# Optimization experiments

Hardware: AMD Instinct MI355X
Metric: run time of the kernel (lower is better)

Reference implementation:

```python
import jax, jax.numpy as jnp
import numpy as np

B, S, E, D = 8, 2048, 1024, 64


def setup_inputs() -> dict:
    key = jax.random.key(0)
    ks = jax.random.split(key, 8)
    x = jax.random.normal(ks[0], (B, S, E), dtype=jnp.float32)
    mask = jax.random.randint(ks[1], (B, S), 0, 2, dtype=jnp.int32)
    # torch.nn.Linear(E, D): weight [D, E], bias [D]; y = x @ W.T + b
    scale = 0.02
    Wq = jax.random.normal(ks[2], (D, E), dtype=jnp.float32) * scale
    bq = jax.random.normal(ks[3], (D,), dtype=jnp.float32) * scale
    Wk = jax.random.normal(ks[4], (D, E), dtype=jnp.float32) * scale
    bk = jax.random.normal(ks[5], (D,), dtype=jnp.float32) * scale
    Wv = jax.random.normal(ks[6], (D, E), dtype=jnp.float32) * scale
    bv = jax.random.normal(ks[7], (D,), dtype=jnp.float32) * scale
    return {"x": x, "mask": mask, "Wq": Wq, "bq": bq, "Wk": Wk, "bk": bk, "Wv": Wv, "bv": bv}


def reference(x, mask, Wq, bq, Wk, bk, Wv, bv):
    # Linear projections: [B,S,E] @ [E,D] -> [B,S,D]
    q = jnp.einsum('bse,de->bsd', x, Wq) + bq
    k = jnp.einsum('bse,de->bsd', x, Wk) + bk
    v = jnp.einsum('bse,de->bsd', x, Wv) + bv
    # scores: [B,S,S]
    scores = jnp.einsum('bid,bjd->bij', q, k) / np.sqrt(D).astype(np.float32)
    # Faithful mask replication: temp_mask[b,i,j] = mask[b,j] if j >= i else 0;
    # positions where temp_mask == 0 are filled with -1e22 (training=True).
    seq = scores.shape[1]
    upper = jnp.triu(jnp.ones((seq, seq), dtype=bool))        # j >= i
    valid = upper[None, :, :] & (mask[:, None, :] != 0)        # [B,S,S]
    scores = jnp.where(valid, scores, jnp.float32(-1e22))
    attn = jax.nn.softmax(scores, axis=-1)
    # out: [B,S,D]
    return jnp.einsum('bij,bjd->bid', attn, v)
```

## Files before the change

kernel.cpp:

```cpp
#include <hip/hip_runtime.h>
#include <hip/hip_bf16.h>

#define NB 8
#define NS 2048
#define NE 1024
#define ND 64

typedef __attribute__((ext_vector_type(8))) short bf16x8;
typedef __attribute__((ext_vector_type(4))) float f32x4;
typedef unsigned short u16;
typedef unsigned long long u64;

#define MFMA(a, b, c) __builtin_amdgcn_mfma_f32_16x16x32_bf16(a, b, c, 0, 0, 0)
#define KEEPB(n) asm volatile("s_waitcnt vmcnt(" #n ")\n\ts_barrier" ::: "memory")

__device__ __forceinline__ u16 f2bf(float f) {
  unsigned int u = __float_as_uint(f);
  u += 0x7fffu + ((u >> 16) & 1u);
  return (u16)(u >> 16);
}
__device__ __forceinline__ unsigned cvt2(float a, float b) {
  __hip_bfloat162 h = __float22bfloat162_rn(float2{a, b});
  return *(unsigned*)&h;
}

__device__ __forceinline__ void alds16(const void* g, void* l) {
  __builtin_amdgcn_global_load_lds(
      (const __attribute__((address_space(1))) unsigned int*)g,
      (__attribute__((address_space(3))) unsigned int*)l, 16, 0, 0);
}

__global__ void k0_prep(const float* __restrict__ Wq, const float* __restrict__ bq,
                        const float* __restrict__ Wk, const float* __restrict__ bk,
                        const float* __restrict__ Wv, const float* __restrict__ bv,
                        u16* __restrict__ Wcat3, float* __restrict__ bcat,
                        float* __restrict__ vmean) {
  int d = blockIdx.x * 256 + threadIdx.x;
  int c = d / 768;
  int rem = d - c * 768;
  int n = rem >> 2;
  int v = rem & 3;
  const float* src = (n < 64) ? (Wq + n * NE) : (n < 128) ? (Wk + (n - 64) * NE)
                                                          : (Wv + (n - 128) * NE);
  const float* sp = src + c * 32 + v * 8;
  float4 a = *(const float4*)sp;
  float4 b = *(const float4*)(sp + 4);
  bf16x8 o;
  o[0] = (short)f2bf(a.x); o[1] = (short)f2bf(a.y);
  o[2] = (short)f2bf(a.z); o[3] = (short)f2bf(a.w);
  o[4] = (short)f2bf(b.x); o[5] = (short)f2bf(b.y);
  o[6] = (short)f2bf(b.z); o[7] = (short)f2bf(b.w);
  *(bf16x8*)&Wcat3[(size_t)d * 8] = o;
  if (blockIdx.x == 0) {
    int t = threadIdx.x;
    if (t < 192) bcat[t] = (t < 64) ? bq[t] : (t < 128) ? bk[t - 64] : bv[t - 128];
    vmean[t] = 0.f;
    vmean[t + 256] = 0.f;
  }
}

__global__ __launch_bounds__(512) void k1_qkv(
    const float* __restrict__ x, const u16* __restrict__ Wcat3,
    const float* __restrict__ bcat, u16* __restrict__ qb,
    u16* __restrict__ kbf2, u16* __restrict__ vtb2, float* __restrict__ vmean) {
  __shared__ float axs[4][1024];
  __shared__ u16 bsb[4][6144];
  const int t = threadIdx.x;
  const int m0 = blockIdx.x * 32;
  const int batch = m0 >> 11;
  const int sl = m0 & (NS - 1);
  const int w = t >> 6;
  const int l = t & 63;
  const int ln = l & 15;
  const int qd = l >> 4;
  const int rg = w & 1;
  const int cg = w >> 1;

  f32x4 zf = {0.f, 0.f, 0.f, 0.f};
  f32x4 acc[3] = {zf, zf, zf};

  auto stage = [&](int c, int buf) {
    if (w < 2) {
      #pragma unroll
      for (int i = 0; i < 2; ++i) {
        int un = w * 128 + i * 64 + l;
        int row = un >> 3;
        int q = (un & 7) ^ (row & 7);
        alds16(x + (size_t)(m0 + row) * NE + c * 32 + q * 4,
               &axs[buf][(w * 128 + i * 64) * 4]);
      }
    } else {
      #pragma unroll
      for (int i = 0; i < 2; ++i) {
        int ub = (w - 2) * 128 + i * 64 + l;
        int n = ub >> 2;
        int v = (ub & 3) ^ ((n ^ (n >> 2)) & 3);
        alds16(Wcat3 + (size_t)c * 6144 + n * 32 + v * 8,
               &bsb[buf][((w - 2) * 128 + i * 64) * 8]);
      }
    }
  };

  auto comp = [&](int buf) {
    const int arow = rg * 16 + ln;
    const int s = arow & 7;
    float4 fa = *(const float4*)&axs[buf][arow * 32 + (((qd * 2) ^ s) << 2)];
    float4 fb = *(const float4*)&axs[buf][arow * 32 + (((qd * 2 + 1) ^ s) << 2)];
    union { bf16x8 v; unsigned u[4]; } A;
    A.u[0] = cvt2(fa.x, fa.y); A.u[1] = cvt2(fa.z, fa.w);
    A.u[2] = cvt2(fb.x, fb.y); A.u[3] = cvt2(fb.z, fb.w);
    #pragma unroll
    for (int nj = 0; nj < 3; ++nj) {
      int n = cg * 48 + nj * 16 + ln;
      int sw = (n ^ (n >> 2)) & 3;
      bf16x8 bb = *(const bf16x8*)&bsb[buf][n * 32 + ((qd ^ sw) << 3)];
      acc[nj] = MFMA(A.v, bb, acc[nj]);
    }
  };

  stage(0, 0);
  stage(1, 1);
  stage(2, 2);
  for (int c = 0; c < 29; ++c) {
    KEEPB(4);
    stage(c + 3, (c + 3) & 3);
    comp(c & 3);
  }
  KEEPB(4); comp(1);
  KEEPB(2); comp(2);
  KEEPB(0); comp(3);

  const float QS = 0.125f;
  #pragma unroll
  for (int nj = 0; nj < 3; ++nj) {
    int n = cg * 48 + nj * 16 + ln;
    float bias = bcat[n];
    int jbase = sl + rg * 16 + qd * 4;
    if (n < 64) {
      #pragma unroll
      for (int r = 0; r < 4; ++r)
        qb[((size_t)batch * NS + jbase + r) * ND + n] = f2bf((acc[nj][r] + bias) * QS);
    } else if (n < 128) {
      int d = n - 64;
      #pragma unroll
      for (int r = 0; r < 4; ++r) {
        int j = jbase + r;
        int pos = (((d >> 3) ^ (j & 7)) << 3) + (d & 7);
        kbf2[((size_t)batch * NS + j) * ND + pos] = f2bf(acc[nj][r] + bias);
      }
    } else {
      int d = n - 128;
      int off = (jbase & ~63) + (((((jbase >> 5) & 1) ^ ((d >> 2) & 1))) << 5) +
                (((((jbase >> 3) & 3) ^ (d & 3))) << 3) + (jbase & 7);
      ushort4 sv;
      sv.x = f2bf(acc[nj][0] + bias); sv.y = f2bf(acc[nj][1] + bias);
      sv.z = f2bf(acc[nj][2] + bias); sv.w = f2bf(acc[nj][3] + bias);
      *(ushort4*)&vtb2[((size_t)batch * ND + d) * NS + off] = sv;
      float psum = acc[nj][0] + acc[nj][1] + acc[nj][2] + acc[nj][3] + 4.f * bias;
      psum += __shfl_xor(psum, 16);
      psum += __shfl_xor(psum, 32);
      if (l < 16) atomicAdd(&vmean[batch * ND + d], psum * (1.f / 2048.f));
    }
  }
}

__global__ __launch_bounds__(512) void k3_attn(
    const u16* __restrict__ qb, const u16* __restrict__ kbf2,
    const u16* __restrict__ vtb2, const int* __restrict__ mask,
    const float* __restrict__ vmean, float* __restrict__ out) {
  __shared__ u16 ks[2][128 * 64];
  __shared__ u16 vs[2][64 * 128];
  __shared__ union {
    u16 ps[8][16 * 40];
    struct { float mb[2][16][68]; float mlb[2][16][16]; } m;
  } ub;

  const int g = blockIdx.x;
  const int b = g & 7;
  const int uu = g >> 3;
  const int tile = (uu & 1) ? (63 - (uu >> 1)) : (uu >> 1);
  const int i0 = tile * 32;
  const int j0f = i0 & ~127;
  const int np = (NS - j0f) >> 7;
  const int t = threadIdx.x;
  const int w = t >> 6;
  const int l = t & 63;
  const int ln = l & 15;
  const int qd = l >> 4;
  const int rg = w & 1;
  const int jg = w >> 1;

  const u16* qp = qb + ((size_t)b * NS + i0 + rg * 16 + ln) * ND + qd * 8;
  bf16x8 aq0 = *(const bf16x8*)qp;
  bf16x8 aq1 = *(const bf16x8*)(qp + 32);

  const u16* kB = kbf2 + (size_t)b * NS * ND;
  const u16* vB = vtb2 + (size_t)b * ND * NS;

  auto stage = [&](int it, int buf) {
    int j0 = j0f + it * 128;
    #pragma unroll
    for (int i = 0; i < 2; ++i) {
      int jl = w * 16 + i * 8;
      alds16(kB + (size_t)(j0 + jl) * ND + l * 8, &ks[buf][jl * 64]);
      int du = w * 2 + i;
      alds16(vB + (size_t)(du * 4 + (l >> 4)) * NS + j0 + (l & 15) * 8,
             &vs[buf][du * 512]);
    }
  };

  f32x4 zf = {0.f, 0.f, 0.f, 0.f};
  f32x4 od[4] = {zf, zf, zf, zf};
  float ls[4] = {0.f, 0.f, 0.f, 0.f};
  const int pvunit = (jg >> 1) * 8 + (((jg & 1) ^ ((ln >> 2) & 1)) << 2) + (qd ^ (ln & 3));

  stage(0, 0);
  int mval = mask[b * NS + j0f + jg * 32 + (l & 31)];

  auto body = [&](int it, bool causal) {
    u64 mv = __ballot(mval != 0);
    __syncthreads();
    if (it + 1 < np) {
      stage(it + 1, (it + 1) & 1);
      mval = mask[b * NS + j0f + (it + 1) * 128 + jg * 32 + (l & 31)];
    }
    const int buf = it & 1;
    const int jb = j0f + it * 128 + jg * 32;

    f32x4 sc[2] = {zf, zf};
    #pragma unroll
    for (int f = 0; f < 2; ++f) {
      const u16* kr = &ks[buf][(jg * 32 + f * 16 + ln) * 64];
      bf16x8 b0 = *(const bf16x8*)&kr[((qd ^ (ln & 7)) * 8)];
      bf16x8 b1 = *(const bf16x8*)&kr[(((4 + qd) ^ (ln & 7)) * 8)];
      sc[f] = MFMA(aq0, b0, sc[f]);
      sc[f] = MFMA(aq1, b1, sc[f]);
    }
    #pragma unroll
    for (int r = 0; r < 4; ++r) {
      const int i = i0 + rg * 16 + qd * 4 + r;
      #pragma unroll
      for (int f = 0; f < 2; ++f) {
        int jl = f * 16 + ln;
        bool ok = (((mv >> jl) & 1ull) != 0) && (!causal || (jb + jl >= i));
        float p = ok ? __expf(sc[f][r]) : 0.f;
        ls[r] += p;
        ub.ps[w][(qd * 4 + r) * 40 + jl] = f2bf(p);
      }
    }
    bf16x8 pa = *(const bf16x8*)&ub.ps[w][ln * 40 + qd * 8];
    #pragma unroll
    for (int gx = 0; gx < 4; ++gx) {
      bf16x8 bv = *(const bf16x8*)&vs[buf][(gx * 16 + ln) * 128 + pvunit * 8];
      od[gx] = MFMA(pa, bv, od[gx]);
    }
  };

  body(0, true);
  for (int it = 1; it < np; ++it) body(it, false);

  __syncthreads();
  #pragma unroll 1
  for (int s = 3; s >= 1; --s) {
    if (jg == s) {
      #pragma unroll
      for (int r = 0; r < 4; ++r) {
        int row = qd * 4 + r;
        #pragma unroll
        for (int gx = 0; gx < 4; ++gx) ub.m.mb[rg][row][gx * 16 + ln] = od[gx][r];
        ub.m.mlb[rg][row][ln] = ls[r];
      }
    }
    __syncthreads();
    if (jg == s - 1) {
      #pragma unroll
      for (int r = 0; r < 4; ++r) {
        int row = qd * 4 + r;
        #pragma unroll
        for (int gx = 0; gx < 4; ++gx) od[gx][r] += ub.m.mb[rg][row][gx * 16 + ln];
        ls[r] += ub.m.mlb[rg][row][ln];
      }
    }
    __syncthreads();
  }

  if (jg == 0) {
    #pragma unroll
    for (int r = 0; r < 4; ++r) {
      #pragma unroll
      for (int o = 1; o < 16; o <<= 1) ls[r] += __shfl_xor(ls[r], o);
      int row = i0 + rg * 16 + qd * 4 + r;
      float* orow = out + ((size_t)b * NS + row) * ND;
      if (ls[r] > 0.f) {
        float inv = 1.f / ls[r];
        #pragma unroll
        for (int gx = 0; gx < 4; ++gx) orow[gx * 16 + ln] = od[gx][r] * inv;
      } else {
        #pragma unroll
        for (int gx = 0; gx < 4; ++gx) orow[gx * 16 + ln] = vmean[b * ND + gx * 16 + ln];
      }
    }
  }
}

extern "C" void kernel_launch(void* const* d_in, const int* in_sizes, int n_in,
                              void* d_out, int out_size, void* d_ws, size_t ws_size,
                              hipStream_t stream) {
  (void)in_sizes; (void)n_in; (void)out_size; (void)ws_size;
  const float* x = (const float*)d_in[0];
  const int* mask = (const int*)d_in[1];
  const float* Wq = (const float*)d_in[2];
  const float* bq = (const float*)d_in[3];
  const float* Wk = (const float*)d_in[4];
  const float* bk = (const float*)d_in[5];
  const float* Wv = (const float*)d_in[6];
  const float* bv = (const float*)d_in[7];
  float* out = (float*)d_out;

  char* ws = (char*)d_ws;
  u16* Wcat3 = (u16*)ws;
  float* bcat = (float*)(ws + 393216);
  float* vmean = (float*)(ws + 394240);
  u16* qb = (u16*)(ws + (1u << 20));
  u16* kbf2 = (u16*)(ws + (3u << 20));
  u16* vtb2 = (u16*)(ws + (5u << 20));

  hipLaunchKernelGGL(k0_prep, dim3(96), dim3(256), 0, stream,
                     Wq, bq, Wk, bk, Wv, bv, Wcat3, bcat, vmean);
  hipLaunchKernelGGL(k1_qkv, dim3(512), dim3(512), 0, stream,
                     x, Wcat3, bcat, qb, kbf2, vtb2, vmean);
  hipLaunchKernelGGL(k3_attn, dim3(512), dim3(512), 0, stream,
                     qb, kbf2, vtb2, mask, vmean, out);
}
```

Baseline: 146.5 us.

## Load K/V fragments directly from global into registers, dropping LDS staging

The attention kernel no longer stages K and V tiles through double-buffered shared memory with async copies and per-iteration barriers. Each wave now loads its own MFMA operand fragments straight from global memory into registers, prefetching K two iterations ahead and V one iteration ahead. The QKV projection writes K and V^T in plain unswizzled layout to match. Launch bounds now request 4 waves per SIMD. This removes LDS traffic and block-wide syncs, but adds redundant global/L2 reads across waves and more register pressure.

```diff
diff --git a/kernel.cpp b/kernel.cpp
--- a/kernel.cpp
+++ b/kernel.cpp
@@ -62,7 +62,7 @@
 __global__ __launch_bounds__(512) void k1_qkv(
     const float* __restrict__ x, const u16* __restrict__ Wcat3,
     const float* __restrict__ bcat, u16* __restrict__ qb,
-    u16* __restrict__ kbf2, u16* __restrict__ vtb2, float* __restrict__ vmean) {
+    u16* __restrict__ kbf, u16* __restrict__ vtb, float* __restrict__ vmean) {
   __shared__ float axs[4][1024];
   __shared__ u16 bsb[4][6144];
   const int t = threadIdx.x;
@@ -143,19 +143,14 @@
     } else if (n < 128) {
       int d = n - 64;
       #pragma unroll
-      for (int r = 0; r < 4; ++r) {
-        int j = jbase + r;
-        int pos = (((d >> 3) ^ (j & 7)) << 3) + (d & 7);
-        kbf2[((size_t)batch * NS + j) * ND + pos] = f2bf(acc[nj][r] + bias);
-      }
+      for (int r = 0; r < 4; ++r)
+        kbf[((size_t)batch * NS + jbase + r) * ND + d] = f2bf(acc[nj][r] + bias);
     } else {
       int d = n - 128;
-      int off = (jbase & ~63) + (((((jbase >> 5) & 1) ^ ((d >> 2) & 1))) << 5) +
-                (((((jbase >> 3) & 3) ^ (d & 3))) << 3) + (jbase & 7);
       ushort4 sv;
       sv.x = f2bf(acc[nj][0] + bias); sv.y = f2bf(acc[nj][1] + bias);
       sv.z = f2bf(acc[nj][2] + bias); sv.w = f2bf(acc[nj][3] + bias);
-      *(ushort4*)&vtb2[((size_t)batch * ND + d) * NS + off] = sv;
+      *(ushort4*)&vtb[((size_t)batch * ND + d) * NS + jbase] = sv;
       float psum = acc[nj][0] + acc[nj][1] + acc[nj][2] + acc[nj][3] + 4.f * bias;
       psum += __shfl_xor(psum, 16);
       psum += __shfl_xor(psum, 32);
@@ -164,12 +159,10 @@
   }
 }
 
-__global__ __launch_bounds__(512) void k3_attn(
-    const u16* __restrict__ qb, const u16* __restrict__ kbf2,
-    const u16* __restrict__ vtb2, const int* __restrict__ mask,
+__global__ __launch_bounds__(512, 4) void k3_attn(
+    const u16* __restrict__ qb, const u16* __restrict__ kbf,
+    const u16* __restrict__ vtb, const int* __restrict__ mask,
     const float* __restrict__ vmean, float* __restrict__ out) {
-  __shared__ u16 ks[2][128 * 64];
-  __shared__ u16 vs[2][64 * 128];
   __shared__ union {
     u16 ps[8][16 * 40];
     struct { float mb[2][16][68]; float mlb[2][16][16]; } m;
@@ -194,70 +187,70 @@
   bf16x8 aq0 = *(const bf16x8*)qp;
   bf16x8 aq1 = *(const bf16x8*)(qp + 32);
 
-  const u16* kB = kbf2 + (size_t)b * NS * ND;
-  const u16* vB = vtb2 + (size_t)b * ND * NS;
-
-  auto stage = [&](int it, int buf) {
-    int j0 = j0f + it * 128;
-    #pragma unroll
-    for (int i = 0; i < 2; ++i) {
-      int jl = w * 16 + i * 8;
-      alds16(kB + (size_t)(j0 + jl) * ND + l * 8, &ks[buf][jl * 64]);
-      int du = w * 2 + i;
-      alds16(vB + (size_t)(du * 4 + (l >> 4)) * NS + j0 + (l & 15) * 8,
-             &vs[buf][du * 512]);
-    }
+  const u16* kB = kbf + (size_t)b * NS * ND;
+  const u16* vB = vtb + (size_t)b * ND * NS;
+  const int mbase = b * NS + j0f + jg * 32 + (l & 31);
+
+  auto ldK = [&](int it, bf16x8 (&kf)[4]) {
+    const u16* p0 = kB + (size_t)(j0f + it * 128 + jg * 32 + ln) * ND + qd * 8;
+    kf[0] = *(const bf16x8*)p0;
+    kf[1] = *(const bf16x8*)(p0 + 32);
+    kf[2] = *(const bf16x8*)(p0 + 16 * ND);
+    kf[3] = *(const bf16x8*)(p0 + 16 * ND + 32);
+  };
+  auto ldV = [&](int it, bf16x8 (&vf)[4]) {
+    const u16* pv = vB + (size_t)ln * NS + j0f + it * 128 + jg * 32 + qd * 8;
+    vf[0] = *(const bf16x8*)pv;
+    vf[1] = *(const bf16x8*)(pv + 16 * NS);
+    vf[2] = *(const bf16x8*)(pv + 32 * NS);
+    vf[3] = *(const bf16x8*)(pv + 48 * NS);
   };
 
   f32x4 zf = {0.f, 0.f, 0.f, 0.f};
   f32x4 od[4] = {zf, zf, zf, zf};
   float ls[4] = {0.f, 0.f, 0.f, 0.f};
-  const int pvunit = (jg >> 1) * 8 + (((jg & 1) ^ ((ln >> 2) & 1)) << 2) + (qd ^ (ln & 3));
-
-  stage(0, 0);
-  int mval = mask[b * NS + j0f + jg * 32 + (l & 31)];
-
-  auto body = [&](int it, bool causal) {
-    u64 mv = __ballot(mval != 0);
-    __syncthreads();
-    if (it + 1 < np) {
-      stage(it + 1, (it + 1) & 1);
-      mval = mask[b * NS + j0f + (it + 1) * 128 + jg * 32 + (l & 31)];
-    }
-    const int buf = it & 1;
+  bf16x8 kfA[4], kfB[4], vf[4];
+  int mvA = 0, mvB = 0;
+
+  ldK(0, kfA); ldV(0, vf);
+  mvA = mask[mbase];
+  if (np > 1) { ldK(1, kfB); mvB = mask[mbase + 128]; }
+
+  auto body = [&](int it, bf16x8 (&kf)[4], int& mslot, bool causal) {
+    u64 mv = __ballot(mslot != 0);
     const int jb = j0f + it * 128 + jg * 32;
-
-    f32x4 sc[2] = {zf, zf};
-    #pragma unroll
-    for (int f = 0; f < 2; ++f) {
-      const u16* kr = &ks[buf][(jg * 32 + f * 16 + ln) * 64];
-      bf16x8 b0 = *(const bf16x8*)&kr[((qd ^ (ln & 7)) * 8)];
-      bf16x8 b1 = *(const bf16x8*)&kr[(((4 + qd) ^ (ln & 7)) * 8)];
-      sc[f] = MFMA(aq0, b0, sc[f]);
-      sc[f] = MFMA(aq1, b1, sc[f]);
-    }
+    f32x4 sc0 = zf, sc1 = zf;
+    sc0 = MFMA(aq0, kf[0], sc0);
+    sc0 = MFMA(aq1, kf[1], sc0);
+    sc1 = MFMA(aq0, kf[2], sc1);
+    sc1 = MFMA(aq1, kf[3], sc1);
+    if (it + 2 < np) { ldK(it + 2, kf); mslot = mask[mbase + (it + 2) * 128]; }
+    const bool ok0 = ((mv >> ln) & 1ull) != 0;
+    const bool ok1 = ((mv >> (16 + ln)) & 1ull) != 0;
     #pragma unroll
     for (int r = 0; r < 4; ++r) {
       const int i = i0 + rg * 16 + qd * 4 + r;
-      #pragma unroll
-      for (int f = 0; f < 2; ++f) {
-        int jl = f * 16 + ln;
-        bool ok = (((mv >> jl) & 1ull) != 0) && (!causal || (jb + jl >= i));
-        float p = ok ? __expf(sc[f][r]) : 0.f;
-        ls[r] += p;
-        ub.ps[w][(qd * 4 + r) * 40 + jl] = f2bf(p);
-      }
+      bool v0 = ok0 && (!causal || (jb + ln >= i));
+      bool v1 = ok1 && (!causal || (jb + 16 + ln >= i));
+      float p0 = v0 ? __expf(sc0[r]) : 0.f;
+      float p1 = v1 ? __expf(sc1[r]) : 0.f;
+      ls[r] += p0 + p1;
+      ub.ps[w][(qd * 4 + r) * 40 + ln] = f2bf(p0);
+      ub.ps[w][(qd * 4 + r) * 40 + 16 + ln] = f2bf(p1);
     }
     bf16x8 pa = *(const bf16x8*)&ub.ps[w][ln * 40 + qd * 8];
-    #pragma unroll
-    for (int gx = 0; gx < 4; ++gx) {
-      bf16x8 bv = *(const bf16x8*)&vs[buf][(gx * 16 + ln) * 128 + pvunit * 8];
-      od[gx] = MFMA(pa, bv, od[gx]);
-    }
-  };
-
-  body(0, true);
-  for (int it = 1; it < np; ++it) body(it, false);
+    od[0] = MFMA(pa, vf[0], od[0]);
+    od[1] = MFMA(pa, vf[1], od[1]);
+    od[2] = MFMA(pa, vf[2], od[2]);
+    od[3] = MFMA(pa, vf[3], od[3]);
+    if (it + 1 < np) ldV(it + 1, vf);
+  };
+
+  body(0, kfA, mvA, true);
+  for (int it = 1; it < np; it += 2) {
+    body(it, kfB, mvB, false);
+    if (it + 1 < np) body(it + 1, kfA, mvA, false);
+  }
 
   __syncthreads();
   #pragma unroll 1
@@ -322,13 +315,13 @@
   float* bcat = (float*)(ws + 393216);
   float* vmean = (float*)(ws + 394240);
   u16* qb = (u16*)(ws + (1u << 20));
-  u16* kbf2 = (u16*)(ws + (3u << 20));
-  u16* vtb2 = (u16*)(ws + (5u << 20));
+  u16* kbf = (u16*)(ws + (3u << 20));
+  u16* vtb = (u16*)(ws + (5u << 20));
 
   hipLaunchKernelGGL(k0_prep, dim3(96), dim3(256), 0, stream,
                      Wq, bq, Wk, bk, Wv, bv, Wcat3, bcat, vmean);
   hipLaunchKernelGGL(k1_qkv, dim3(512), dim3(512), 0, stream,
-                     x, Wcat3, bcat, qb, kbf2, vtb2, vmean);
+                     x, Wcat3, bcat, qb, kbf, vtb, vmean);
   hipLaunchKernelGGL(k3_attn, dim3(512), dim3(512), 0, stream,
-                     qb, kbf2, vtb2, mask, vmean, out);
-}
+                     qb, kbf, vtb, mask, vmean, out);
+}
```

Result: slower. 175.3 us (+19.7%).

## Double QKV projection row tile to 64 and deepen the load pipeline to five stages

Applied to the files above, without the earlier changes.

The QKV projection kernel now processes 64 rows of x per block instead of 32, with each wave computing a 16x96 output slab using six MFMAs. The concatenated weight tile is now staged once per 64 rows instead of once per 32, which halves weight traffic into LDS. The async global-to-LDS ring grows from four to five buffers, with per-wave vmcnt waits matched to each wave's load count. Only half as many blocks launch, and LDS per block grows to about 100 KB, which limits occupancy and may leave some CUs idle.

```diff
diff --git a/kernel.cpp b/kernel.cpp
--- a/kernel.cpp
+++ b/kernel.cpp
@@ -12,7 +12,6 @@
 typedef unsigned long long u64;
 
 #define MFMA(a, b, c) __builtin_amdgcn_mfma_f32_16x16x32_bf16(a, b, c, 0, 0, 0)
-#define KEEPB(n) asm volatile("s_waitcnt vmcnt(" #n ")\n\ts_barrier" ::: "memory")
 
 __device__ __forceinline__ u16 f2bf(float f) {
   unsigned int u = __float_as_uint(f);
@@ -59,45 +58,39 @@
   }
 }
 
-__global__ __launch_bounds__(512) void k1_qkv(
+__global__ __launch_bounds__(512, 2) void k1_qkv(
     const float* __restrict__ x, const u16* __restrict__ Wcat3,
     const float* __restrict__ bcat, u16* __restrict__ qb,
     u16* __restrict__ kbf2, u16* __restrict__ vtb2, float* __restrict__ vmean) {
-  __shared__ float axs[4][1024];
-  __shared__ u16 bsb[4][6144];
+  __shared__ float axs[5][2048];
+  __shared__ u16 bsb[5][6144];
   const int t = threadIdx.x;
-  const int m0 = blockIdx.x * 32;
+  const int m0 = blockIdx.x * 64;
   const int batch = m0 >> 11;
   const int sl = m0 & (NS - 1);
   const int w = t >> 6;
   const int l = t & 63;
   const int ln = l & 15;
   const int qd = l >> 4;
-  const int rg = w & 1;
-  const int cg = w >> 1;
+  const int rg = w >> 1;
+  const int cg = w & 1;
 
   f32x4 zf = {0.f, 0.f, 0.f, 0.f};
-  f32x4 acc[3] = {zf, zf, zf};
+  f32x4 acc[6] = {zf, zf, zf, zf, zf, zf};
 
   auto stage = [&](int c, int buf) {
-    if (w < 2) {
-      #pragma unroll
-      for (int i = 0; i < 2; ++i) {
-        int un = w * 128 + i * 64 + l;
-        int row = un >> 3;
-        int q = (un & 7) ^ (row & 7);
-        alds16(x + (size_t)(m0 + row) * NE + c * 32 + q * 4,
-               &axs[buf][(w * 128 + i * 64) * 4]);
-      }
-    } else {
-      #pragma unroll
-      for (int i = 0; i < 2; ++i) {
-        int ub = (w - 2) * 128 + i * 64 + l;
-        int n = ub >> 2;
-        int v = (ub & 3) ^ ((n ^ (n >> 2)) & 3);
-        alds16(Wcat3 + (size_t)c * 6144 + n * 32 + v * 8,
-               &bsb[buf][((w - 2) * 128 + i * 64) * 8]);
-      }
+    {
+      int row = w * 8 + (l >> 3);
+      int gch = (l & 7) ^ (row & 7);
+      alds16(x + (size_t)(m0 + row) * NE + c * 32 + gch * 4, &axs[buf][w * 8 * 32]);
+    }
+    int nb = (w < 4) ? 2 : 1;
+    int j0 = (w < 4) ? 2 * w : 4 + w;
+    for (int i = 0; i < nb; ++i) {
+      int j = j0 + i;
+      int n = j * 16 + (l >> 2);
+      int v = (l & 3) ^ ((n ^ (n >> 2)) & 3);
+      alds16(Wcat3 + (size_t)c * 6144 + n * 32 + v * 8, &bsb[buf][j * 16 * 32]);
     }
   };
 
@@ -110,30 +103,38 @@
     A.u[0] = cvt2(fa.x, fa.y); A.u[1] = cvt2(fa.z, fa.w);
     A.u[2] = cvt2(fb.x, fb.y); A.u[3] = cvt2(fb.z, fb.w);
     #pragma unroll
-    for (int nj = 0; nj < 3; ++nj) {
-      int n = cg * 48 + nj * 16 + ln;
+    for (int nj = 0; nj < 6; ++nj) {
+      int n = cg * 96 + nj * 16 + ln;
       int sw = (n ^ (n >> 2)) & 3;
       bf16x8 bb = *(const bf16x8*)&bsb[buf][n * 32 + ((qd ^ sw) << 3)];
       acc[nj] = MFMA(A.v, bb, acc[nj]);
     }
   };
 
-  stage(0, 0);
-  stage(1, 1);
-  stage(2, 2);
+  stage(0, 0); stage(1, 1); stage(2, 2); stage(3, 3);
+  #pragma unroll
   for (int c = 0; c < 29; ++c) {
-    KEEPB(4);
-    stage(c + 3, (c + 3) & 3);
-    comp(c & 3);
-  }
-  KEEPB(4); comp(1);
-  KEEPB(2); comp(2);
-  KEEPB(0); comp(3);
+    if (w < 4) asm volatile("s_waitcnt vmcnt(9)" ::: "memory");
+    else       asm volatile("s_waitcnt vmcnt(6)" ::: "memory");
+    asm volatile("s_barrier" ::: "memory");
+    if (c + 4 < 32) stage(c + 4, (c + 4) % 5);
+    comp(c % 5);
+  }
+  if (w < 4) asm volatile("s_waitcnt vmcnt(6)" ::: "memory");
+  else       asm volatile("s_waitcnt vmcnt(4)" ::: "memory");
+  asm volatile("s_barrier" ::: "memory");
+  comp(4);
+  if (w < 4) asm volatile("s_waitcnt vmcnt(3)" ::: "memory");
+  else       asm volatile("s_waitcnt vmcnt(2)" ::: "memory");
+  asm volatile("s_barrier" ::: "memory");
+  comp(0);
+  asm volatile("s_waitcnt vmcnt(0)\n\ts_barrier" ::: "memory");
+  comp(1);
 
   const float QS = 0.125f;
   #pragma unroll
-  for (int nj = 0; nj < 3; ++nj) {
-    int n = cg * 48 + nj * 16 + ln;
+  for (int nj = 0; nj < 6; ++nj) {
+    int n = cg * 96 + nj * 16 + ln;
     float bias = bcat[n];
     int jbase = sl + rg * 16 + qd * 4;
     if (n < 64) {
@@ -327,7 +328,7 @@
 
   hipLaunchKernelGGL(k0_prep, dim3(96), dim3(256), 0, stream,
                      Wq, bq, Wk, bk, Wv, bv, Wcat3, bcat, vmean);
-  hipLaunchKernelGGL(k1_qkv, dim3(512), dim3(512), 0, stream,
+  hipLaunchKernelGGL(k1_qkv, dim3(256), dim3(512), 0, stream,
                      x, Wcat3, bcat, qb, kbf2, vtb2, vmean);
   hipLaunchKernelGGL(k3_attn, dim3(512), dim3(512), 0, stream,
                      qb, kbf2, vtb2, mask, vmean, out);
```

New measurement: 151.3 us. 1.03x slower.
